# Performance work log

Measured on AMD Instinct MI355X. Metric: run time of the kernel, lower is better.

## Reference

```python
import jax, jax.numpy as jnp
import numpy as np

B, THETA_DIM, Y_DIM, OUT_DIM, WIDTH, NUM_BLOCKS, MULT = 16384, 64, 16, 256, 1024, 4, 2
EPS = 1e-5


def setup_inputs() -> dict:
    key = jax.random.key(0)
    ks = jax.random.split(key, 16)
    hid = MULT * WIDTH
    in_dim = THETA_DIM + 1 + Y_DIM
    inp = {
        "theta_n": jax.random.normal(ks[0], (B, THETA_DIM), jnp.float32),
        "lambda_n": jax.random.normal(ks[1], (B, 1), jnp.float32),
        "y_oh": jax.random.uniform(ks[2], (B, Y_DIM), jnp.float32),
        # input layer
        "W_in": jax.random.normal(ks[3], (in_dim, WIDTH), jnp.float32) * 0.02,
        "b_in": jnp.zeros((WIDTH,), jnp.float32),
        # stacked ResBlockLN params [num_blocks, ...]
        "ln_g": jnp.ones((NUM_BLOCKS, WIDTH), jnp.float32),
        "ln_b": jnp.zeros((NUM_BLOCKS, WIDTH), jnp.float32),
        "w1": jax.random.normal(ks[4], (NUM_BLOCKS, WIDTH, hid), jnp.float32) * 0.02,
        "b1": jnp.zeros((NUM_BLOCKS, hid), jnp.float32),
        "w2": jax.random.normal(ks[5], (NUM_BLOCKS, hid, WIDTH), jnp.float32) * 0.02,
        "b2": jnp.zeros((NUM_BLOCKS, WIDTH), jnp.float32),
        "res_scale": jnp.full((NUM_BLOCKS,), 0.1, jnp.float32),
        # per-class heads stacked [y_dim, width, out_dim]
        "Wh": jax.random.normal(ks[6], (Y_DIM, WIDTH, OUT_DIM), jnp.float32) * 0.02,
        "bh": jnp.zeros((Y_DIM, OUT_DIM), jnp.float32),
    }
    return inp


def _layernorm(x, g, b):
    mu = jnp.mean(x, axis=-1, keepdims=True)
    var = jnp.mean(jnp.square(x - mu), axis=-1, keepdims=True)
    return (x - mu) * jax.lax.rsqrt(var + EPS) * g + b


def reference(theta_n, lambda_n, y_oh, W_in, b_in, ln_g, ln_b, w1, b1, w2, b2, res_scale, Wh, bh):
    x = jnp.concatenate([theta_n, lambda_n, y_oh], axis=1)  # [B, theta+1+y]
    h = jax.nn.gelu(x @ W_in + b_in, approximate=False)      # [B, width]
    for i in range(NUM_BLOCKS):
        z = _layernorm(h, ln_g[i], ln_b[i])
        z = jax.nn.silu(z @ w1[i] + b1[i])
        z = z @ w2[i] + b2[i]
        h = h + res_scale[i] * z
    y_int = jnp.argmax(y_oh, axis=1)                         # [B]
    # compute all heads, then per-sample gather (argmax-routed head)
    all_out = jnp.einsum("bd,kdo->bko", h, Wh) + bh          # [B, y_dim, out_dim]
    out = jnp.take_along_axis(all_out, y_int[:, None, None], axis=1)[:, 0, :]
    return out
```

## Files before the change

kernel.cpp:

```cpp
#include <hip/hip_runtime.h>
#include <hip/hip_bf16.h>
#include <cstdint>
#include <cstddef>

#define B_ROWS 16384
#define WIDTH  1024
#define HID    2048
#define NBLK   4
#define YDIM   16
#define OUTD   256
#define KIN    128
#define MAXM_PER_CLASS 4096

typedef __attribute__((ext_vector_type(8))) short short8;
typedef __attribute__((ext_vector_type(4))) float f32x4;

__device__ __forceinline__ unsigned short f2bf(float f) {
    union { float f; uint32_t u; } v; v.f = f;
    uint32_t u = v.u;
    uint32_t r = (u + 0x7FFFu + ((u >> 16) & 1u)) >> 16;
    return (unsigned short)r;
}

__device__ __forceinline__ void gload_lds16(const void* g, void* l) {
    __builtin_amdgcn_global_load_lds(
        (const __attribute__((address_space(1))) void*)g,
        (__attribute__((address_space(3))) void*)l, 16, 0, 0);
}

__global__ __launch_bounds__(256)
void prep_x_k(const float* __restrict__ theta, const float* __restrict__ lam,
              const float* __restrict__ yoh, unsigned short* __restrict__ xb)
{
    int tid = threadIdx.x;
    int row = blockIdx.x * 2 + (tid >> 7);
    int j = tid & 127;
    float v;
    if (j < 64)       v = theta[(size_t)row * 64 + j];
    else if (j == 64) v = lam[row];
    else if (j < 81)  v = yoh[(size_t)row * 16 + (j - 65)];
    else              v = 0.f;
    xb[(size_t)row * KIN + j] = f2bf(v);
}

__global__ __launch_bounds__(256)
void bucket_k(const float* __restrict__ yoh, int* __restrict__ counts,
              int* __restrict__ bucket)
{
    __shared__ int cnt_lds[16];
    __shared__ int base_lds[16];
    int tid = threadIdx.x;
    if (tid < 16) cnt_lds[tid] = 0;
    __syncthreads();
    int row = blockIdx.x * 256 + tid;
    const float4* yr = (const float4*)(yoh + (size_t)row * 16);
    int best = 0; float bv = -3.0e38f;
    #pragma unroll
    for (int p = 0; p < 4; ++p) {
        float4 v = yr[p];
        if (v.x > bv) { bv = v.x; best = p * 4 + 0; }
        if (v.y > bv) { bv = v.y; best = p * 4 + 1; }
        if (v.z > bv) { bv = v.z; best = p * 4 + 2; }
        if (v.w > bv) { bv = v.w; best = p * 4 + 3; }
    }
    int mypos = atomicAdd(&cnt_lds[best], 1);
    __syncthreads();
    if (tid < 16) base_lds[tid] = atomicAdd(&counts[tid * 32], cnt_lds[tid]);
    __syncthreads();
    int pos = base_lds[best] + mypos;
    if (pos < MAXM_PER_CLASS) bucket[best * MAXM_PER_CLASS + pos] = row;
}

__global__ __launch_bounds__(256)
void tcvt_k(const float* __restrict__ src, unsigned short* __restrict__ dst,
            int R, int C, int RP)
{
    int b = blockIdx.z;
    src += (size_t)b * R * C;
    dst += (size_t)b * C * RP;
    __shared__ float tile[32][33];
    int tx = threadIdx.x & 31, ty = threadIdx.x >> 5;
    int c0 = blockIdx.x * 32, r0 = blockIdx.y * 32;
    #pragma unroll
    for (int p = 0; p < 4; ++p) {
        int r = r0 + p * 8 + ty;
        float v = (r < R) ? src[(size_t)r * C + c0 + tx] : 0.f;
        tile[p * 8 + ty][tx] = v;
    }
    __syncthreads();
    #pragma unroll
    for (int p = 0; p < 4; ++p) {
        int c = c0 + p * 8 + ty;
        dst[(size_t)c * RP + r0 + tx] = f2bf(tile[tx][p * 8 + ty]);
    }
}

__global__ __launch_bounds__(256)
void ln_k(const float* __restrict__ h, const float* __restrict__ g,
          const float* __restrict__ bb, unsigned short* __restrict__ z)
{
    int row = blockIdx.x;
    int t = threadIdx.x;
    const float4 v = ((const float4*)(h + (size_t)row * WIDTH))[t];
    float s  = v.x + v.y + v.z + v.w;
    float s2 = v.x * v.x + v.y * v.y + v.z * v.z + v.w * v.w;
    #pragma unroll
    for (int off = 32; off > 0; off >>= 1) {
        s  += __shfl_down(s, off);
        s2 += __shfl_down(s2, off);
    }
    __shared__ float red[8];
    int wv = t >> 6;
    if ((t & 63) == 0) { red[wv] = s; red[4 + wv] = s2; }
    __syncthreads();
    float st = 0.f, s2t = 0.f;
    #pragma unroll
    for (int i = 0; i < 4; ++i) { st += red[i]; s2t += red[4 + i]; }
    float mu  = st * (1.f / 1024.f);
    float var = s2t * (1.f / 1024.f) - mu * mu;
    float rs  = rsqrtf(var + 1e-5f);
    float4 gg  = ((const float4*)g)[t];
    float4 bbv = ((const float4*)bb)[t];
    ushort4 o;
    o.x = f2bf((v.x - mu) * rs * gg.x + bbv.x);
    o.y = f2bf((v.y - mu) * rs * gg.y + bbv.y);
    o.z = f2bf((v.z - mu) * rs * gg.z + bbv.z);
    o.w = f2bf((v.w - mu) * rs * gg.w + bbv.w);
    ((ushort4*)(z + (size_t)row * WIDTH))[t] = o;
}

template<int EPI>
__global__ __launch_bounds__(512, 2)
void gemm256_k(const short* __restrict__ A, const short* __restrict__ BT,
               const float* __restrict__ bias,
               float* __restrict__ Cf, unsigned short* __restrict__ Cb,
               const float* __restrict__ rs_ptr, int rs_idx, int writeHb,
               int N, int K, int ntN)
{
    __shared__ short lsA[2][256 * 64];
    __shared__ short lsB[2][256 * 64];

    int tid = threadIdx.x;
    int w = tid >> 6, lane = tid & 63;

    int nwg = gridDim.x;
    int wg  = blockIdx.x;
    int cpx = nwg >> 3;
    int swz = (wg & 7) * cpx + (wg >> 3);
    int bm = swz / ntN, bn = swz % ntN;

    const int wm = w >> 2, wn = w & 3;
    const int lr8 = lane >> 3;
    const int ls8 = lane & 7;
    const int nkt = K >> 6;

    f32x4 acc[8][4];
    #pragma unroll
    for (int i = 0; i < 8; ++i)
        #pragma unroll
        for (int j = 0; j < 4; ++j) acc[i][j] = (f32x4)(0.f);

    auto STAGE = [&](int buf, int kt) {
        #pragma unroll
        for (int c = 0; c < 4; ++c) {
            int r  = c * 64 + w * 8 + lr8;
            int sg = ls8 ^ (r & 7);
            const short* ga = A + (size_t)(bm * 256 + r) * K + (size_t)kt * 64 + sg * 8;
            gload_lds16(ga, &lsA[buf][(c * 64 + w * 8) * 64]);
        }
        #pragma unroll
        for (int c = 0; c < 4; ++c) {
            int r  = c * 64 + w * 8 + lr8;
            int sg = ls8 ^ (r & 7);
            const short* gb = BT + (size_t)(bn * 256 + r) * K + (size_t)kt * 64 + sg * 8;
            gload_lds16(gb, &lsB[buf][(c * 64 + w * 8) * 64]);
        }
    };

    STAGE(0, 0);
    asm volatile("s_waitcnt vmcnt(0)" ::: "memory");
    __builtin_amdgcn_s_barrier();

    int cur = 0;
    for (int kt = 0; kt < nkt; ++kt) {
        if (kt + 1 < nkt) STAGE(cur ^ 1, kt + 1);

        #pragma unroll
        for (int ks = 0; ks < 2; ++ks) {
            short8 af[8], bf[4];
            int s = ks * 4 + (lane >> 4);
            #pragma unroll
            for (int m = 0; m < 8; ++m) {
                int r = wm * 128 + m * 16 + (lane & 15);
                af[m] = *(const short8*)&lsA[cur][r * 64 + (s ^ (r & 7)) * 8];
            }
            #pragma unroll
            for (int n = 0; n < 4; ++n) {
                int r = wn * 64 + n * 16 + (lane & 15);
                bf[n] = *(const short8*)&lsB[cur][r * 64 + (s ^ (r & 7)) * 8];
            }
            __builtin_amdgcn_s_setprio(1);
            #pragma unroll
            for (int m = 0; m < 8; ++m)
                #pragma unroll
                for (int n = 0; n < 4; ++n)
                    acc[m][n] = __builtin_amdgcn_mfma_f32_16x16x32_bf16(af[m], bf[n], acc[m][n], 0, 0, 0);
            __builtin_amdgcn_s_setprio(0);
        }

        asm volatile("s_waitcnt vmcnt(0)" ::: "memory");
        __builtin_amdgcn_s_barrier();
        cur ^= 1;
    }

    float rscale = (EPI == 2) ? rs_ptr[rs_idx] : 0.f;
    #pragma unroll
    for (int m = 0; m < 8; ++m) {
        #pragma unroll
        for (int reg = 0; reg < 4; ++reg) {
            int lr = wm * 128 + m * 16 + (lane >> 4) * 4 + reg;
            #pragma unroll
            for (int n = 0; n < 4; ++n) {
                int lc = wn * 64 + n * 16 + (lane & 15);
                float v = acc[m][n][reg];
                size_t idx = ((size_t)bm * 256 + lr) * (size_t)N + bn * 256 + lc;
                float x = v + bias[bn * 256 + lc];
                if (EPI == 1) {
                    Cb[idx] = f2bf(x / (1.f + __expf(-x)));
                } else {
                    float hv = Cf[idx] + rscale * x;
                    Cf[idx] = hv;
                    if (writeHb) Cb[idx] = f2bf(hv);
                }
            }
        }
    }
}

template<int EPI>
__global__ __launch_bounds__(256)
void gemm_k(const short* __restrict__ A, const short* __restrict__ BT,
            const float* __restrict__ bias,
            float* __restrict__ Cf,
            const int* __restrict__ counts, const int* __restrict__ bucket,
            float* __restrict__ outp,
            int N, int K, int ntN)
{
    __shared__ short lsA[2][128 * 64];
    __shared__ short lsB[2][128 * 64];
    __shared__ int rowsLds[128];

    int tid = threadIdx.x;
    int w = tid >> 6, lane = tid & 63;

    int bm = 0, bn = 0, m0 = 0, cnt = 0;
    if (EPI == 3) {
        int cls = blockIdx.z;
        cnt = counts[cls * 32];
        if (cnt > MAXM_PER_CLASS) cnt = MAXM_PER_CLASS;
        m0 = blockIdx.y * 128;
        if (m0 >= cnt) return;
        bn = blockIdx.x;
        if (tid < 128) rowsLds[tid] = bucket[cls * MAXM_PER_CLASS + m0 + tid];
        __syncthreads();
        BT   += (size_t)cls * OUTD * WIDTH;
        bias += cls * OUTD;
    } else {
        int nwg = gridDim.x;
        int wg  = blockIdx.x;
        int cpx = nwg >> 3;
        int swz = (wg & 7) * cpx + (wg >> 3);
        bm = swz / ntN; bn = swz % ntN;
    }

    const int sr = lane >> 3;
    const int ss = lane & 7;
    const int wm = w >> 1, wn = w & 1;
    const int nkt = K >> 6;

    f32x4 acc[4][4];
    #pragma unroll
    for (int i = 0; i < 4; ++i)
        #pragma unroll
        for (int j = 0; j < 4; ++j) acc[i][j] = (f32x4)(0.f);

    auto STAGE = [&](int buf, int kt) {
        #pragma unroll
        for (int c = 0; c < 4; ++c) {
            int r  = w * 32 + c * 8 + sr;
            int sg = ss ^ (r & 7);
            long grow = (EPI == 3) ? (long)rowsLds[r] : ((long)bm * 128 + r);
            const short* ga = A + (size_t)grow * K + (size_t)kt * 64 + sg * 8;
            gload_lds16(ga, &lsA[buf][(w * 32 + c * 8) * 64]);
        }
        #pragma unroll
        for (int c = 0; c < 4; ++c) {
            int r  = w * 32 + c * 8 + sr;
            int sg = ss ^ (r & 7);
            const short* gb = BT + (size_t)(bn * 128 + r) * K + (size_t)kt * 64 + sg * 8;
            gload_lds16(gb, &lsB[buf][(w * 32 + c * 8) * 64]);
        }
    };

    STAGE(0, 0);
    asm volatile("s_waitcnt vmcnt(0)" ::: "memory");
    __builtin_amdgcn_s_barrier();

    int cur = 0;
    for (int kt = 0; kt < nkt; ++kt) {
        if (kt + 1 < nkt) STAGE(cur ^ 1, kt + 1);

        #pragma unroll
        for (int ks = 0; ks < 2; ++ks) {
            short8 af[4], bf[4];
            #pragma unroll
            for (int m = 0; m < 4; ++m) {
                int r = wm * 64 + m * 16 + (lane & 15);
                int s = ks * 4 + (lane >> 4);
                af[m] = *(const short8*)&lsA[cur][r * 64 + (s ^ (r & 7)) * 8];
            }
            #pragma unroll
            for (int n = 0; n < 4; ++n) {
                int r = wn * 64 + n * 16 + (lane & 15);
                int s = ks * 4 + (lane >> 4);
                bf[n] = *(const short8*)&lsB[cur][r * 64 + (s ^ (r & 7)) * 8];
            }
            __builtin_amdgcn_s_setprio(1);
            #pragma unroll
            for (int m = 0; m < 4; ++m)
                #pragma unroll
                for (int n = 0; n < 4; ++n)
                    acc[m][n] = __builtin_amdgcn_mfma_f32_16x16x32_bf16(af[m], bf[n], acc[m][n], 0, 0, 0);
            __builtin_amdgcn_s_setprio(0);
        }

        asm volatile("s_waitcnt vmcnt(0)" ::: "memory");
        __builtin_amdgcn_s_barrier();
        cur ^= 1;
    }

    #pragma unroll
    for (int m = 0; m < 4; ++m) {
        #pragma unroll
        for (int reg = 0; reg < 4; ++reg) {
            int lr = wm * 64 + m * 16 + (lane >> 4) * 4 + reg;
            #pragma unroll
            for (int n = 0; n < 4; ++n) {
                int lc = wn * 64 + n * 16 + (lane & 15);
                float v = acc[m][n][reg];
                if (EPI == 0) {
                    size_t idx = ((size_t)bm * 128 + lr) * (size_t)N + bn * 128 + lc;
                    float x = v + bias[bn * 128 + lc];
                    Cf[idx] = 0.5f * x * (1.f + erff(x * 0.70710678118f));
                } else {
                    if (m0 + lr < cnt) {
                        int orow = rowsLds[lr];
                        int oc = bn * 128 + lc;
                        outp[(size_t)orow * OUTD + oc] = v + bias[oc];
                    }
                }
            }
        }
    }
}

extern "C" void kernel_launch(void* const* d_in, const int* in_sizes, int n_in,
                              void* d_out, int out_size, void* d_ws, size_t ws_size,
                              hipStream_t stream)
{
    const float* theta = (const float*)d_in[0];
    const float* lam   = (const float*)d_in[1];
    const float* yoh   = (const float*)d_in[2];
    const float* W_in  = (const float*)d_in[3];
    const float* b_in  = (const float*)d_in[4];
    const float* ln_g  = (const float*)d_in[5];
    const float* ln_b  = (const float*)d_in[6];
    const float* w1    = (const float*)d_in[7];
    const float* b1    = (const float*)d_in[8];
    const float* w2    = (const float*)d_in[9];
    const float* b2    = (const float*)d_in[10];
    const float* rsc   = (const float*)d_in[11];
    const float* Wh    = (const float*)d_in[12];
    const float* bh    = (const float*)d_in[13];
    float* out = (float*)d_out;

    char* p = (char*)d_ws;
    auto alloc = [&](size_t bytes) -> char* {
        char* r = p; p += (bytes + 255) & ~(size_t)255; return r;
    };
    float*          h    = (float*)         alloc((size_t)B_ROWS * WIDTH * 4);
    unsigned short* hb   = (unsigned short*)alloc((size_t)B_ROWS * WIDTH * 2);
    unsigned short* z    = (unsigned short*)alloc((size_t)B_ROWS * WIDTH * 2);
    unsigned short* t    = (unsigned short*)alloc((size_t)B_ROWS * HID * 2);
    unsigned short* xb   = (unsigned short*)alloc((size_t)B_ROWS * KIN * 2);
    unsigned short* w1T  = (unsigned short*)alloc((size_t)NBLK * HID * WIDTH * 2);
    unsigned short* w2T  = (unsigned short*)alloc((size_t)NBLK * WIDTH * HID * 2);
    unsigned short* WhT  = (unsigned short*)alloc((size_t)YDIM * OUTD * WIDTH * 2);
    unsigned short* WiT  = (unsigned short*)alloc((size_t)WIDTH * KIN * 2);
    int*            bucket = (int*)alloc((size_t)YDIM * MAXM_PER_CLASS * 4);
    int*            counts = (int*)alloc(16 * 32 * 4);

    hipMemsetAsync(bucket, 0, (size_t)YDIM * MAXM_PER_CLASS * 4, stream);
    hipMemsetAsync(counts, 0, 16 * 32 * 4, stream);

    prep_x_k<<<B_ROWS / 2, 256, 0, stream>>>(theta, lam, yoh, xb);
    bucket_k<<<B_ROWS / 256, 256, 0, stream>>>(yoh, counts, bucket);

    tcvt_k<<<dim3(WIDTH / 32, KIN / 32, 1),    256, 0, stream>>>(W_in, WiT, 81,   WIDTH, KIN);
    tcvt_k<<<dim3(HID / 32,   WIDTH / 32, 4),  256, 0, stream>>>(w1,   w1T, WIDTH, HID,  WIDTH);
    tcvt_k<<<dim3(WIDTH / 32, HID / 32, 4),    256, 0, stream>>>(w2,   w2T, HID,  WIDTH, HID);
    tcvt_k<<<dim3(OUTD / 32,  WIDTH / 32, 16), 256, 0, stream>>>(Wh,   WhT, WIDTH, OUTD, WIDTH);

    gemm_k<0><<<(B_ROWS / 128) * (WIDTH / 128), 256, 0, stream>>>(
        (const short*)xb, (const short*)WiT, b_in, h,
        nullptr, nullptr, nullptr, WIDTH, KIN, WIDTH / 128);

    for (int i = 0; i < NBLK; ++i) {
        ln_k<<<B_ROWS, 256, 0, stream>>>(h, ln_g + i * WIDTH, ln_b + i * WIDTH, z);
        gemm256_k<1><<<(B_ROWS / 256) * (HID / 256), 512, 0, stream>>>(
            (const short*)z, (const short*)(w1T + (size_t)i * HID * WIDTH), b1 + i * HID,
            nullptr, t, nullptr, 0, 0, HID, WIDTH, HID / 256);
        gemm256_k<2><<<(B_ROWS / 256) * (WIDTH / 256), 512, 0, stream>>>(
            (const short*)t, (const short*)(w2T + (size_t)i * WIDTH * HID), b2 + i * WIDTH,
            h, hb, rsc, i, (i == NBLK - 1) ? 1 : 0, WIDTH, HID, WIDTH / 256);
    }

    gemm_k<3><<<dim3(OUTD / 128, MAXM_PER_CLASS / 128, YDIM), 256, 0, stream>>>(
        (const short*)hb, (const short*)WhT, bh, nullptr,
        counts, bucket, out, OUTD, WIDTH, OUTD / 128);

    (void)in_sizes; (void)n_in; (void)out_size; (void)ws_size; (void)rsc;
}
```

Measured before the change: 1.013 ms.

## Restructure 256x256 GEMM main loop into quadrant-staged fine-grained pipeline

The big-tile GEMM main loop is rewritten so that A and B half-tiles are staged separately and interleaved with four quadrant MFMA phases per k-step. The loop is unrolled by two k-tiles, with explicit vmcnt(4) partial waits and extra barriers. The aim is to overlap global-to-LDS loads with compute more finely than a single full-tile prefetch with a vmcnt(0) wait. In exchange there are many more barriers per iteration, and buffer-reuse correctness now depends on careful ordering. The code assumes an even number of k-tiles.

Measured after the change: 988.7 us. 1.02x faster.

```diff
diff --git a/kernel.cpp b/kernel.cpp
--- a/kernel.cpp
+++ b/kernel.cpp
@@ -14,6 +14,12 @@
 
 typedef __attribute__((ext_vector_type(8))) short short8;
 typedef __attribute__((ext_vector_type(4))) float f32x4;
+
+#define FENCE() asm volatile("" ::: "memory")
+#define BAR()   do { FENCE(); __builtin_amdgcn_s_barrier(); FENCE(); } while (0)
+#define LGKM0() asm volatile("s_waitcnt lgkmcnt(0)" ::: "memory")
+#define VM4()   asm volatile("s_waitcnt vmcnt(4)" ::: "memory")
+#define VM0()   asm volatile("s_waitcnt vmcnt(0)" ::: "memory")
 
 __device__ __forceinline__ unsigned short f2bf(float f) {
     union { float f; uint32_t u; } v; v.f = f;
@@ -153,6 +159,7 @@
     const int lr8 = lane >> 3;
     const int ls8 = lane & 7;
     const int nkt = K >> 6;
+    const int nit = nkt >> 1;
 
     f32x4 acc[8][4];
     #pragma unroll
@@ -160,57 +167,129 @@
         #pragma unroll
         for (int j = 0; j < 4; ++j) acc[i][j] = (f32x4)(0.f);
 
-    auto STAGE = [&](int buf, int kt) {
-        #pragma unroll
-        for (int c = 0; c < 4; ++c) {
-            int r  = c * 64 + w * 8 + lr8;
+    auto STAGE_A = [&](int buf, int h, int kt) {
+        #pragma unroll
+        for (int c = 0; c < 2; ++c) {
+            int r  = h * 128 + c * 64 + w * 8 + lr8;
             int sg = ls8 ^ (r & 7);
-            const short* ga = A + (size_t)(bm * 256 + r) * K + (size_t)kt * 64 + sg * 8;
-            gload_lds16(ga, &lsA[buf][(c * 64 + w * 8) * 64]);
-        }
-        #pragma unroll
-        for (int c = 0; c < 4; ++c) {
-            int r  = c * 64 + w * 8 + lr8;
+            const short* g = A + (size_t)(bm * 256 + r) * K + (size_t)kt * 64 + sg * 8;
+            gload_lds16(g, &lsA[buf][(h * 128 + c * 64 + w * 8) * 64]);
+        }
+    };
+    auto STAGE_B = [&](int buf, int h, int kt) {
+        #pragma unroll
+        for (int c = 0; c < 2; ++c) {
+            int r  = h * 128 + c * 64 + w * 8 + lr8;
             int sg = ls8 ^ (r & 7);
-            const short* gb = BT + (size_t)(bn * 256 + r) * K + (size_t)kt * 64 + sg * 8;
-            gload_lds16(gb, &lsB[buf][(c * 64 + w * 8) * 64]);
-        }
-    };
-
-    STAGE(0, 0);
-    asm volatile("s_waitcnt vmcnt(0)" ::: "memory");
-    __builtin_amdgcn_s_barrier();
-
-    int cur = 0;
-    for (int kt = 0; kt < nkt; ++kt) {
-        if (kt + 1 < nkt) STAGE(cur ^ 1, kt + 1);
-
-        #pragma unroll
-        for (int ks = 0; ks < 2; ++ks) {
-            short8 af[8], bf[4];
-            int s = ks * 4 + (lane >> 4);
-            #pragma unroll
-            for (int m = 0; m < 8; ++m) {
+            const short* g = BT + (size_t)(bn * 256 + r) * K + (size_t)kt * 64 + sg * 8;
+            gload_lds16(g, &lsB[buf][(h * 128 + c * 64 + w * 8) * 64]);
+        }
+    };
+
+    short8 aL[4][2], aH[4][2], bL[2][2], bH[2][2];
+
+    auto RD_AL = [&](int buf) {
+        #pragma unroll
+        for (int m = 0; m < 4; ++m)
+            #pragma unroll
+            for (int ks = 0; ks < 2; ++ks) {
                 int r = wm * 128 + m * 16 + (lane & 15);
-                af[m] = *(const short8*)&lsA[cur][r * 64 + (s ^ (r & 7)) * 8];
-            }
-            #pragma unroll
-            for (int n = 0; n < 4; ++n) {
+                int s = ks * 4 + (lane >> 4);
+                aL[m][ks] = *(const short8*)&lsA[buf][r * 64 + (s ^ (r & 7)) * 8];
+            }
+    };
+    auto RD_AH = [&](int buf) {
+        #pragma unroll
+        for (int m = 0; m < 4; ++m)
+            #pragma unroll
+            for (int ks = 0; ks < 2; ++ks) {
+                int r = wm * 128 + 64 + m * 16 + (lane & 15);
+                int s = ks * 4 + (lane >> 4);
+                aH[m][ks] = *(const short8*)&lsA[buf][r * 64 + (s ^ (r & 7)) * 8];
+            }
+    };
+    auto RD_BL = [&](int buf) {
+        #pragma unroll
+        for (int n = 0; n < 2; ++n)
+            #pragma unroll
+            for (int ks = 0; ks < 2; ++ks) {
                 int r = wn * 64 + n * 16 + (lane & 15);
-                bf[n] = *(const short8*)&lsB[cur][r * 64 + (s ^ (r & 7)) * 8];
-            }
-            __builtin_amdgcn_s_setprio(1);
-            #pragma unroll
-            for (int m = 0; m < 8; ++m)
+                int s = ks * 4 + (lane >> 4);
+                bL[n][ks] = *(const short8*)&lsB[buf][r * 64 + (s ^ (r & 7)) * 8];
+            }
+    };
+    auto RD_BH = [&](int buf) {
+        #pragma unroll
+        for (int n = 0; n < 2; ++n)
+            #pragma unroll
+            for (int ks = 0; ks < 2; ++ks) {
+                int r = wn * 64 + 32 + n * 16 + (lane & 15);
+                int s = ks * 4 + (lane >> 4);
+                bH[n][ks] = *(const short8*)&lsB[buf][r * 64 + (s ^ (r & 7)) * 8];
+            }
+    };
+
+    auto MM = [&](short8 (&a)[4][2], short8 (&b)[2][2], int mo, int no) {
+        __builtin_amdgcn_s_setprio(1);
+        #pragma unroll
+        for (int ks = 0; ks < 2; ++ks)
+            #pragma unroll
+            for (int m = 0; m < 4; ++m)
                 #pragma unroll
-                for (int n = 0; n < 4; ++n)
-                    acc[m][n] = __builtin_amdgcn_mfma_f32_16x16x32_bf16(af[m], bf[n], acc[m][n], 0, 0, 0);
-            __builtin_amdgcn_s_setprio(0);
-        }
-
-        asm volatile("s_waitcnt vmcnt(0)" ::: "memory");
-        __builtin_amdgcn_s_barrier();
-        cur ^= 1;
+                for (int n = 0; n < 2; ++n)
+                    acc[mo + m][no + n] = __builtin_amdgcn_mfma_f32_16x16x32_bf16(
+                        a[m][ks], b[n][ks], acc[mo + m][no + n], 0, 0, 0);
+        __builtin_amdgcn_s_setprio(0);
+    };
+
+    STAGE_B(0, 0, 0); STAGE_B(0, 1, 0);
+    STAGE_A(0, 0, 0); STAGE_A(0, 1, 0);
+    STAGE_B(1, 0, 1); STAGE_B(1, 1, 1);
+    VM4(); BAR();
+
+    for (int it = 0; it < nit; ++it) {
+        int T = it * 2;
+        bool nl = (it + 1 < nit);
+        RD_AL(0); RD_BL(0);
+        STAGE_A(1, 0, T + 1);
+        BAR(); LGKM0();
+        MM(aL, bL, 0, 0);
+        BAR();
+        RD_BH(0);
+        STAGE_A(1, 1, T + 1);
+        BAR(); LGKM0();
+        MM(aL, bH, 0, 2);
+        BAR();
+        RD_AH(0);
+        if (nl) STAGE_B(0, 0, T + 2);
+        BAR(); LGKM0();
+        MM(aH, bL, 4, 0);
+        BAR();
+        if (nl) STAGE_B(0, 1, T + 2);
+        BAR(); LGKM0();
+        MM(aH, bH, 4, 2);
+        if (nl) { VM4(); } else { VM0(); }
+        BAR();
+        RD_AL(1); RD_BL(1);
+        if (nl) STAGE_A(0, 0, T + 2);
+        BAR(); LGKM0();
+        MM(aL, bL, 0, 0);
+        BAR();
+        RD_BH(1);
+        if (nl) STAGE_A(0, 1, T + 2);
+        BAR(); LGKM0();
+        MM(aL, bH, 0, 2);
+        BAR();
+        RD_AH(1);
+        if (nl) STAGE_B(1, 0, T + 3);
+        BAR(); LGKM0();
+        MM(aH, bL, 4, 0);
+        BAR();
+        if (nl) STAGE_B(1, 1, T + 3);
+        BAR(); LGKM0();
+        MM(aH, bH, 4, 2);
+        if (nl) { VM4(); }
+        BAR();
     }
 
     float rscale = (EPI == 2) ? rs_ptr[rs_idx] : 0.f;
@@ -303,7 +382,7 @@
     };
 
     STAGE(0, 0);
-    asm volatile("s_waitcnt vmcnt(0)" ::: "memory");
+    VM0();
     __builtin_amdgcn_s_barrier();
 
     int cur = 0;
@@ -334,7 +413,7 @@
             __builtin_amdgcn_s_setprio(0);
         }
 
-        asm volatile("s_waitcnt vmcnt(0)" ::: "memory");
+        VM0();
         __builtin_amdgcn_s_barrier();
         cur ^= 1;
     }
```

## Use 128x256 tiles with triple-buffered LDS pipeline in residual-block GEMMs

Applied to the files above, without the earlier changes.

Replaces the 256x256 double-buffered GEMM with a 128x256 tile and a three-stage LDS ring buffer. Loads run two k-tiles ahead and are waited on with a partial vmcnt, so one barrier per iteration replaces the full drain. Halving the M tile doubles the grid and cuts the accumulator registers, but lowers arithmetic intensity per workgroup and adds more reloads of the B operand.

Result: slower. 1.176 ms (+16.1%).

```diff
diff --git a/kernel.cpp b/kernel.cpp
--- a/kernel.cpp
+++ b/kernel.cpp
@@ -14,6 +14,11 @@
 
 typedef __attribute__((ext_vector_type(8))) short short8;
 typedef __attribute__((ext_vector_type(4))) float f32x4;
+
+#define FENCE() asm volatile("" ::: "memory")
+#define BAR()   do { FENCE(); __builtin_amdgcn_s_barrier(); FENCE(); } while (0)
+#define VM6()   asm volatile("s_waitcnt vmcnt(6)" ::: "memory")
+#define VM0()   asm volatile("s_waitcnt vmcnt(0)" ::: "memory")
 
 __device__ __forceinline__ unsigned short f2bf(float f) {
     union { float f; uint32_t u; } v; v.f = f;
@@ -131,14 +136,14 @@
 
 template<int EPI>
 __global__ __launch_bounds__(512, 2)
-void gemm256_k(const short* __restrict__ A, const short* __restrict__ BT,
-               const float* __restrict__ bias,
-               float* __restrict__ Cf, unsigned short* __restrict__ Cb,
-               const float* __restrict__ rs_ptr, int rs_idx, int writeHb,
-               int N, int K, int ntN)
-{
-    __shared__ short lsA[2][256 * 64];
-    __shared__ short lsB[2][256 * 64];
+void gemm3_k(const short* __restrict__ A, const short* __restrict__ BT,
+             const float* __restrict__ bias,
+             float* __restrict__ Cf, unsigned short* __restrict__ Cb,
+             const float* __restrict__ rs_ptr, int rs_idx, int writeHb,
+             int N, int K, int ntN)
+{
+    __shared__ short lsA[3][128 * 64];
+    __shared__ short lsB[3][256 * 64];
 
     int tid = threadIdx.x;
     int w = tid >> 6, lane = tid & 63;
@@ -150,80 +155,81 @@
     int bm = swz / ntN, bn = swz % ntN;
 
     const int wm = w >> 2, wn = w & 3;
-    const int lr8 = lane >> 3;
-    const int ls8 = lane & 7;
+    const int sr = lane >> 3;
+    const int ss = lane & 7;
     const int nkt = K >> 6;
 
-    f32x4 acc[8][4];
-    #pragma unroll
-    for (int i = 0; i < 8; ++i)
+    f32x4 acc[4][4];
+    #pragma unroll
+    for (int i = 0; i < 4; ++i)
         #pragma unroll
         for (int j = 0; j < 4; ++j) acc[i][j] = (f32x4)(0.f);
 
     auto STAGE = [&](int buf, int kt) {
         #pragma unroll
+        for (int c = 0; c < 2; ++c) {
+            int r  = c * 64 + w * 8 + sr;
+            int sg = ss ^ (r & 7);
+            const short* ga = A + (size_t)(bm * 128 + r) * K + (size_t)kt * 64 + sg * 8;
+            gload_lds16(ga, &lsA[buf][(c * 64 + w * 8) * 64]);
+        }
+        #pragma unroll
         for (int c = 0; c < 4; ++c) {
-            int r  = c * 64 + w * 8 + lr8;
-            int sg = ls8 ^ (r & 7);
-            const short* ga = A + (size_t)(bm * 256 + r) * K + (size_t)kt * 64 + sg * 8;
-            gload_lds16(ga, &lsA[buf][(c * 64 + w * 8) * 64]);
-        }
-        #pragma unroll
-        for (int c = 0; c < 4; ++c) {
-            int r  = c * 64 + w * 8 + lr8;
-            int sg = ls8 ^ (r & 7);
+            int r  = c * 64 + w * 8 + sr;
+            int sg = ss ^ (r & 7);
             const short* gb = BT + (size_t)(bn * 256 + r) * K + (size_t)kt * 64 + sg * 8;
             gload_lds16(gb, &lsB[buf][(c * 64 + w * 8) * 64]);
         }
     };
 
     STAGE(0, 0);
-    asm volatile("s_waitcnt vmcnt(0)" ::: "memory");
-    __builtin_amdgcn_s_barrier();
+    STAGE(1, 1);
 
     int cur = 0;
     for (int kt = 0; kt < nkt; ++kt) {
-        if (kt + 1 < nkt) STAGE(cur ^ 1, kt + 1);
+        if (kt + 1 < nkt) { VM6(); } else { VM0(); }
+        BAR();
+        int nxt = cur + 2; if (nxt >= 3) nxt -= 3;
+        if (kt + 2 < nkt) STAGE(nxt, kt + 2);
 
         #pragma unroll
         for (int ks = 0; ks < 2; ++ks) {
-            short8 af[8], bf[4];
-            int s = ks * 4 + (lane >> 4);
-            #pragma unroll
-            for (int m = 0; m < 8; ++m) {
-                int r = wm * 128 + m * 16 + (lane & 15);
+            short8 af[4], bf[4];
+            #pragma unroll
+            for (int m = 0; m < 4; ++m) {
+                int r = wm * 64 + m * 16 + (lane & 15);
+                int s = ks * 4 + (lane >> 4);
                 af[m] = *(const short8*)&lsA[cur][r * 64 + (s ^ (r & 7)) * 8];
             }
             #pragma unroll
             for (int n = 0; n < 4; ++n) {
                 int r = wn * 64 + n * 16 + (lane & 15);
+                int s = ks * 4 + (lane >> 4);
                 bf[n] = *(const short8*)&lsB[cur][r * 64 + (s ^ (r & 7)) * 8];
             }
             __builtin_amdgcn_s_setprio(1);
             #pragma unroll
-            for (int m = 0; m < 8; ++m)
+            for (int m = 0; m < 4; ++m)
                 #pragma unroll
                 for (int n = 0; n < 4; ++n)
                     acc[m][n] = __builtin_amdgcn_mfma_f32_16x16x32_bf16(af[m], bf[n], acc[m][n], 0, 0, 0);
             __builtin_amdgcn_s_setprio(0);
         }
 
-        asm volatile("s_waitcnt vmcnt(0)" ::: "memory");
-        __builtin_amdgcn_s_barrier();
-        cur ^= 1;
+        cur = (cur == 2) ? 0 : cur + 1;
     }
 
     float rscale = (EPI == 2) ? rs_ptr[rs_idx] : 0.f;
     #pragma unroll
-    for (int m = 0; m < 8; ++m) {
+    for (int m = 0; m < 4; ++m) {
         #pragma unroll
         for (int reg = 0; reg < 4; ++reg) {
-            int lr = wm * 128 + m * 16 + (lane >> 4) * 4 + reg;
+            int lr = wm * 64 + m * 16 + (lane >> 4) * 4 + reg;
             #pragma unroll
             for (int n = 0; n < 4; ++n) {
                 int lc = wn * 64 + n * 16 + (lane & 15);
                 float v = acc[m][n][reg];
-                size_t idx = ((size_t)bm * 256 + lr) * (size_t)N + bn * 256 + lc;
+                size_t idx = ((size_t)bm * 128 + lr) * (size_t)N + bn * 256 + lc;
                 float x = v + bias[bn * 256 + lc];
                 if (EPI == 1) {
                     Cb[idx] = f2bf(x / (1.f + __expf(-x)));
@@ -303,7 +309,7 @@
     };
 
     STAGE(0, 0);
-    asm volatile("s_waitcnt vmcnt(0)" ::: "memory");
+    VM0();
     __builtin_amdgcn_s_barrier();
 
     int cur = 0;
@@ -334,7 +340,7 @@
             __builtin_amdgcn_s_setprio(0);
         }
 
-        asm volatile("s_waitcnt vmcnt(0)" ::: "memory");
+        VM0();
         __builtin_amdgcn_s_barrier();
         cur ^= 1;
     }
@@ -417,10 +423,10 @@
 
     for (int i = 0; i < NBLK; ++i) {
         ln_k<<<B_ROWS, 256, 0, stream>>>(h, ln_g + i * WIDTH, ln_b + i * WIDTH, z);
-        gemm256_k<1><<<(B_ROWS / 256) * (HID / 256), 512, 0, stream>>>(
+        gemm3_k<1><<<(B_ROWS / 128) * (HID / 256), 512, 0, stream>>>(
             (const short*)z, (const short*)(w1T + (size_t)i * HID * WIDTH), b1 + i * HID,
             nullptr, t, nullptr, 0, 0, HID, WIDTH, HID / 256);
-        gemm256_k<2><<<(B_ROWS / 256) * (WIDTH / 256), 512, 0, stream>>>(
+        gemm3_k<2><<<(B_ROWS / 128) * (WIDTH / 256), 512, 0, stream>>>(
             (const short*)t, (const short*)(w2T + (size_t)i * WIDTH * HID), b2 + i * WIDTH,
             h, hb, rsc, i, (i == NBLK - 1) ? 1 : 0, WIDTH, HID, WIDTH / 256);
     }
```
